# Kernel tuning notes

Measured on AMD Instinct MI355X. Metric: run time of the kernel, lower is better.

The kernel has to match this reference:

```python
import math
import jax, jax.numpy as jnp
import numpy as np

D_MODEL = 1024
N_HEADS = 16
D_FF = 4096
B = 4
T = 1024  # tgt len
S = 1024  # src len
EPS = 1e-6


def _linear_params(key, d_in, d_out):
    kw, kb = jax.random.split(key)
    w = jax.random.normal(kw, (d_out, d_in), dtype=jnp.float32) * 0.02
    b = jax.random.normal(kb, (d_out,), dtype=jnp.float32) * 0.02
    return w, b


def setup_inputs() -> dict:
    key = jax.random.key(0)
    ks = jax.random.split(key, 16)
    x = jax.random.normal(ks[0], (B, T, D_MODEL), dtype=jnp.float32)
    memory = jax.random.normal(ks[1], (B, S, D_MODEL), dtype=jnp.float32)
    # causal [B, T, T] mask (dim==3 branch) and padding [B, S] mask (dim==2 branch)
    tgt_mask = jnp.broadcast_to(jnp.tril(jnp.ones((T, T), dtype=jnp.int32)), (B, T, T))
    src_mask = jnp.ones((B, S), dtype=jnp.int32)
    inp = {"x": x, "memory": memory, "tgt_mask": tgt_mask, "src_mask": src_mask}
    names = ["sa_wq", "sa_wk", "sa_wv", "sa_wo", "ca_wq", "ca_wk", "ca_wv", "ca_wo"]
    for i, n in enumerate(names):
        w, b = _linear_params(ks[2 + i], D_MODEL, D_MODEL)
        inp[n] = w
        inp[n.replace("w", "b")] = b
    inp["ff_w1"], inp["ff_b1"] = _linear_params(ks[10], D_MODEL, D_FF)
    inp["ff_w2"], inp["ff_b2"] = _linear_params(ks[11], D_FF, D_MODEL)
    for i, n in enumerate(["ln1", "ln2", "ln3"]):
        inp[n + "_w"] = jnp.ones((D_MODEL,), dtype=jnp.float32)
        inp[n + "_b"] = jnp.zeros((D_MODEL,), dtype=jnp.float32)
    return inp


def layernorm(x, w, b):
    # torch-faithful: unbiased std (N-1), eps added to std (not variance)
    mean = jnp.mean(x, axis=-1, keepdims=True)
    d = x - mean
    std = jnp.sqrt(jnp.sum(d * d, axis=-1, keepdims=True) / (x.shape[-1] - 1))
    return w * d / (std + EPS) + b


def mha(q_in, kv_in, mask, wq, bq, wk, bk, wv, bv, wo, bo):
    Bb, Tq, D = q_in.shape
    Tk = kv_in.shape[1]
    dk = D // N_HEADS
    if mask.ndim == 2:
        mask4 = mask[:, None, None, :]
    else:
        mask4 = mask[:, None, :, :]
    q = (q_in @ wq.T + bq).reshape(Bb, Tq, N_HEADS, dk).transpose(0, 2, 1, 3)
    k = (kv_in @ wk.T + bk).reshape(Bb, Tk, N_HEADS, dk).transpose(0, 2, 1, 3)
    v = (kv_in @ wv.T + bv).reshape(Bb, Tk, N_HEADS, dk).transpose(0, 2, 1, 3)
    scores = jnp.einsum("bhqd,bhkd->bhqk", q, k) / math.sqrt(dk)
    scores = jnp.where(mask4 == 0, jnp.float32(-1e9), scores)
    attn = jax.nn.softmax(scores, axis=-1)
    out = jnp.einsum("bhqk,bhkd->bhqd", attn, v)
    out = out.transpose(0, 2, 1, 3).reshape(Bb, Tq, D)
    return out @ wo.T + bo


def reference(x, memory, tgt_mask, src_mask,
              sa_wq, sa_bq, sa_wk, sa_bk, sa_wv, sa_bv, sa_wo, sa_bo,
              ca_wq, ca_bq, ca_wk, ca_bk, ca_wv, ca_bv, ca_wo, ca_bo,
              ff_w1, ff_b1, ff_w2, ff_b2,
              ln1_w, ln1_b, ln2_w, ln2_b, ln3_w, ln3_b):
    # pre-norm decoder block (norm_first=True), dropout=0 (eval)
    h = layernorm(x, ln1_w, ln1_b)
    x = x + mha(h, h, tgt_mask, sa_wq, sa_bq, sa_wk, sa_bk, sa_wv, sa_bv, sa_wo, sa_bo)
    h = layernorm(x, ln2_w, ln2_b)
    x = x + mha(h, memory, src_mask, ca_wq, ca_bq, ca_wk, ca_bk, ca_wv, ca_bv, ca_wo, ca_bo)
    h = layernorm(x, ln3_w, ln3_b)
    x = x + (jax.nn.relu(h @ ff_w1.T + ff_b1) @ ff_w2.T + ff_b2)
    return x
```

## Files before the change

kernel.cpp:

```cpp
#include <hip/hip_runtime.h>
#include <hip/hip_bf16.h>

typedef unsigned short u16;
typedef __attribute__((ext_vector_type(4))) float f32x4;
typedef __attribute__((ext_vector_type(8))) short s16x8;
typedef __attribute__((ext_vector_type(4))) short s16x4;
typedef __attribute__((ext_vector_type(8))) __bf16 bf16x8;

#define NTOK 4096
#define DMODEL 1024
#define DFF 4096
#define NH 16
#define TSEQ 1024


__device__ __forceinline__ u16 f2bu(float f) {
  unsigned int u = __float_as_uint(f);
  unsigned int r = (u + 0x7FFFu + ((u >> 16) & 1u)) >> 16;
  return (u16)r;
}

__device__ __forceinline__ f32x4 mfma16(s16x8 a, s16x8 b, f32x4 c) {
  return __builtin_amdgcn_mfma_f32_16x16x32_bf16((bf16x8)a, (bf16x8)b, c, 0, 0, 0);
}

__device__ __forceinline__ void gload16(const u16* g, u16* l) {
  __builtin_amdgcn_global_load_lds(
      (const __attribute__((address_space(1))) unsigned int*)g,
      (__attribute__((address_space(3))) unsigned int*)l, 16, 0, 0);
}

__device__ __forceinline__ s16x8 ldfrag(const u16* p) {
  s16x4 lo = *(const s16x4*)p;
  s16x4 hi = *(const s16x4*)(p + 16);
  s16x8 r;
  r[0] = lo[0]; r[1] = lo[1]; r[2] = lo[2]; r[3] = lo[3];
  r[4] = hi[0]; r[5] = hi[1]; r[6] = hi[2]; r[7] = hi[3];
  return r;
}

__device__ __forceinline__ s16x8 ld8s(const u16* t, int row, int eoff) {
  int rx = row & 7;
  const u16* p1 = t + row * 64 + ((((eoff >> 3) ^ rx) << 3) | (eoff & 7));
  const u16* p2 = t + row * 64 + (((((eoff + 16) >> 3) ^ rx) << 3) | (eoff & 7));
  s16x4 lo = *(const s16x4*)p1;
  s16x4 hi = *(const s16x4*)p2;
  s16x8 r;
  r[0] = lo[0]; r[1] = lo[1]; r[2] = lo[2]; r[3] = lo[3];
  r[4] = hi[0]; r[5] = hi[1]; r[6] = hi[2]; r[7] = hi[3];
  return r;
}

__device__ __forceinline__ s16x8 ld16s(const u16* t, int row, int ch) {
  return *(const s16x8*)(t + row * 64 + ((ch ^ (row & 7)) << 3));
}


struct F2B {
  const float* s[11];
  u16* d[11];
};

__global__ __launch_bounds__(256) void f2b_all(F2B a) {
  int bid = blockIdx.x;
  int seg, boff;
  if (bid < 8192) { seg = bid >> 10; boff = bid & 1023; }
  else { int j = bid - 8192; seg = 8 + (j >> 12); boff = j & 4095; }
  size_t i = ((size_t)boff * 256 + threadIdx.x) * 4;
  float4 v = *(const float4*)(a.s[seg] + i);
  ushort4 o = make_ushort4(f2bu(v.x), f2bu(v.y), f2bu(v.z), f2bu(v.w));
  *(ushort4*)(a.d[seg] + i) = o;
}


__global__ __launch_bounds__(256) void ln_kernel(const float* __restrict__ x,
                                                 const float* __restrict__ w,
                                                 const float* __restrict__ b,
                                                 u16* __restrict__ out) {
  int row = blockIdx.x;
  int t = threadIdx.x;
  const float* xr = x + (size_t)row * DMODEL;
  float4 v = *(const float4*)(xr + t * 4);
  float s = v.x + v.y + v.z + v.w;
#pragma unroll
  for (int off = 1; off < 64; off <<= 1) s += __shfl_xor(s, off);
  __shared__ float red[8];
  int wid = t >> 6, lane = t & 63;
  if (lane == 0) red[wid] = s;
  __syncthreads();
  float mean = (red[0] + red[1] + red[2] + red[3]) * (1.0f / 1024.0f);
  float dx = v.x - mean, dy = v.y - mean, dz = v.z - mean, dw = v.w - mean;
  float ss = dx * dx + dy * dy + dz * dz + dw * dw;
#pragma unroll
  for (int off = 1; off < 64; off <<= 1) ss += __shfl_xor(ss, off);
  if (lane == 0) red[4 + wid] = ss;
  __syncthreads();
  float sst = red[4] + red[5] + red[6] + red[7];
  float inv = 1.0f / (sqrtf(sst / 1023.0f) + 1e-6f);
  float4 wv = *(const float4*)(w + t * 4);
  float4 bv = *(const float4*)(b + t * 4);
  ushort4 o = make_ushort4(f2bu(wv.x * dx * inv + bv.x), f2bu(wv.y * dy * inv + bv.y),
                           f2bu(wv.z * dz * inv + bv.z), f2bu(wv.w * dw * inv + bv.w));
  *(ushort4*)(out + (size_t)row * DMODEL + t * 4) = o;
}


template <int MODE, bool RELU>
__global__ __launch_bounds__(512) void gemm_bt(const u16* __restrict__ A,
                                               const u16* __restrict__ W,
                                               const float* __restrict__ b0,
                                               const float* __restrict__ b1,
                                               const float* __restrict__ b2,
                                               const float* resid, void* outp,
                                               int M, int N, int K, int gx) {
  __shared__ u16 As[2][128 * 64];
  __shared__ u16 Bs[2][128 * 64];
  const int nwg = gridDim.x;
  const int qch = nwg >> 3;
  const int bid = blockIdx.x;
  const int wg = (bid & 7) * qch + (bid >> 3);
  const int bx = wg % gx, by = wg / gx;
  const int m0 = by * 128, n0 = bx * 128;
  const int tid = threadIdx.x;
  const int wid = tid >> 6, lane = tid & 63;
  const int wr = wid >> 2, wc = wid & 3;
  const int lhi = lane >> 4, llo = lane & 15;
  f32x4 acc[4][2] = {};
  const int sr = tid >> 3, sc = tid & 7;
  const int srcoff = (sc ^ (sr & 7)) << 3;

  auto stage = [&](int kk, int buf) {
    const u16* Ap = A + (size_t)(m0 + sr) * K + kk + srcoff;
    gload16(Ap, &As[buf][tid * 8]);
    gload16(Ap + (size_t)64 * K, &As[buf][4096 + tid * 8]);
    const u16* Wp = W + (size_t)(n0 + sr) * K + kk + srcoff;
    gload16(Wp, &Bs[buf][tid * 8]);
    gload16(Wp + (size_t)64 * K, &Bs[buf][4096 + tid * 8]);
  };

  stage(0, 0);
  __syncthreads();

  for (int k0 = 0; k0 < K; k0 += 64) {
    int cur = (k0 >> 6) & 1;
    if (k0 + 64 < K) stage(k0 + 64, cur ^ 1);
#pragma unroll
    for (int ks8 = 0; ks8 < 8; ks8 += 4) {
      s16x8 af[4], bfr[2];
#pragma unroll
      for (int f = 0; f < 4; f++) af[f] = ld16s(&As[cur][0], wr * 64 + f * 16 + llo, ks8 + lhi);
#pragma unroll
      for (int g = 0; g < 2; g++) bfr[g] = ld16s(&Bs[cur][0], wc * 32 + g * 16 + llo, ks8 + lhi);
#pragma unroll
      for (int f = 0; f < 4; f++)
#pragma unroll
        for (int g = 0; g < 2; g++) acc[f][g] = mfma16(af[f], bfr[g], acc[f][g]);
    }
    __syncthreads();
  }

  const float* bias;
  if (MODE == 2) {
    int bs = n0 >> 10;
    bias = (bs == 0) ? b0 : ((bs == 1) ? b1 : b2);
  } else {
    bias = b0;
  }

#pragma unroll
  for (int fm = 0; fm < 4; fm++) {
#pragma unroll
    for (int fn = 0; fn < 2; fn++) {
      int c = n0 + wc * 32 + fn * 16 + llo;
      float bv = (MODE == 2) ? bias[c & 1023] : bias[c];
#pragma unroll
      for (int i = 0; i < 4; i++) {
        int r = m0 + wr * 64 + fm * 16 + lhi * 4 + i;
        float v = acc[fm][fn][i] + bv;
        if (resid) v += resid[(size_t)r * N + c];
        if (RELU) v = fmaxf(v, 0.0f);
        if (MODE == 0) {
          ((float*)outp)[(size_t)r * N + c] = v;
        } else if (MODE == 1) {
          ((u16*)outp)[(size_t)r * N + c] = f2bu(v);
        } else {
          int buf = c >> 10, cc = c & 1023;
          int bb = r >> 10, t = r & 1023, hh = cc >> 6, d = cc & 63;
          ((u16*)outp)[(size_t)buf * 4194304 +
                       (((size_t)(bb * NH + hh)) * TSEQ + t) * 64 + d] = f2bu(v);
        }
      }
    }
  }
}


template <bool CAUSAL>
__global__ __launch_bounds__(256) void attn_kernel(const u16* __restrict__ Qg,
                                                   const u16* __restrict__ Kg,
                                                   const u16* __restrict__ Vg,
                                                   u16* __restrict__ Og) {
  int bh = blockIdx.y;
  int b = bh >> 4, h = bh & 15;
  int q0 = blockIdx.x * 64;
  int tid = threadIdx.x, wid = tid >> 6, lane = tid & 63;
  int lhi = lane >> 4, llo = lane & 15;
  __shared__ u16 Ks[2][4096];
  __shared__ u16 Vs[2][4096];

  int qrow = q0 + wid * 16 + llo;
  const u16* qp = Qg + ((size_t)bh * TSEQ + qrow) * 64;
  s16x8 qf0 = ldfrag(qp + lhi * 4);
  s16x8 qf1 = ldfrag(qp + 32 + lhi * 4);

  f32x4 oacc[4] = {};
  float mrun = -3.0e38f, lrun = 0.0f;
  const size_t kvbase = (size_t)bh * TSEQ * 64;
  const int nt = (CAUSAL ? (q0 + 64) : TSEQ) >> 6;

  const int kr = tid >> 3, kc = tid & 7;
  const int ksrc = (kc ^ (kr & 7)) << 3;
  const int vkv = tid & 63, vd0 = (tid >> 6) * 8;
  s16x8 vr0, vr1;

  auto stageK = [&](int s0, int buf) {
    const u16* kb = Kg + kvbase + (size_t)s0 * 64;
    gload16(kb + (size_t)kr * 64 + ksrc, &Ks[buf][tid * 8]);
    gload16(kb + (size_t)(32 + kr) * 64 + ksrc, &Ks[buf][2048 + tid * 8]);
  };
  auto loadV = [&](int s0) {
    const u16* vb = Vg + kvbase + (size_t)(s0 + vkv) * 64;
    vr0 = *(const s16x8*)(vb + vd0);
    vr1 = *(const s16x8*)(vb + vd0 + 32);
  };
  auto writeV = [&](int buf) {
#pragma unroll
    for (int j = 0; j < 8; j++) {
      int d = vd0 + j;
      Vs[buf][d * 64 + ((((vkv >> 3) ^ (d & 7)) << 3) | (vkv & 7))] = (u16)vr0[j];
      int d2 = d + 32;
      Vs[buf][d2 * 64 + ((((vkv >> 3) ^ (d2 & 7)) << 3) | (vkv & 7))] = (u16)vr1[j];
    }
  };

  stageK(0, 0);
  loadV(0);
  writeV(0);
  __syncthreads();

  for (int t = 0; t < nt; ++t) {
    int cur = t & 1;
    if (t + 1 < nt) {
      stageK((t + 1) * 64, cur ^ 1);
      loadV((t + 1) * 64);
    }
    int s0 = t * 64;

    f32x4 sacc[4] = {};
#pragma unroll
    for (int g = 0; g < 4; g++) {
      int row = g * 16 + llo;
      sacc[g] = mfma16(ld8s(&Ks[cur][0], row, lhi * 4), qf0, sacc[g]);
      sacc[g] = mfma16(ld8s(&Ks[cur][0], row, 32 + lhi * 4), qf1, sacc[g]);
    }

    float sv[16];
    float pmax = -3.0e38f;
#pragma unroll
    for (int g = 0; g < 4; g++)
#pragma unroll
      for (int i = 0; i < 4; i++) {
        float sc = sacc[g][i] * 0.125f;
        if (CAUSAL) {
          int kv = s0 + g * 16 + lhi * 4 + i;
          if (kv > qrow) sc = -1.0e9f;
        }
        sv[g * 4 + i] = sc;
        pmax = fmaxf(pmax, sc);
      }
    pmax = fmaxf(pmax, __shfl_xor(pmax, 16));
    pmax = fmaxf(pmax, __shfl_xor(pmax, 32));
    float mnew = fmaxf(mrun, pmax);
    float alpha = __expf(mrun - mnew);
    float pv[16];
    float ls = 0.0f;
#pragma unroll
    for (int j = 0; j < 16; j++) {
      float p = __expf(sv[j] - mnew);
      pv[j] = p;
      ls += p;
    }
    ls += __shfl_xor(ls, 16);
    ls += __shfl_xor(ls, 32);
    lrun = lrun * alpha + ls;
    mrun = mnew;
#pragma unroll
    for (int g = 0; g < 4; g++) {
      oacc[g][0] *= alpha; oacc[g][1] *= alpha;
      oacc[g][2] *= alpha; oacc[g][3] *= alpha;
    }
    s16x8 pf[2];
#pragma unroll
    for (int kk = 0; kk < 2; kk++)
#pragma unroll
      for (int i2 = 0; i2 < 8; i2++)
        pf[kk][i2] = (short)f2bu(pv[(kk * 2 + (i2 >> 2)) * 4 + (i2 & 3)]);
#pragma unroll
    for (int dg = 0; dg < 4; dg++) {
      int row = dg * 16 + llo;
      oacc[dg] = mfma16(ld8s(&Vs[cur][0], row, lhi * 4), pf[0], oacc[dg]);
      oacc[dg] = mfma16(ld8s(&Vs[cur][0], row, 32 + lhi * 4), pf[1], oacc[dg]);
    }

    if (t + 1 < nt) writeV(cur ^ 1);
    __syncthreads();
  }

  float inv = 1.0f / lrun;
  u16* orow = Og + (size_t)(b * TSEQ + qrow) * DMODEL + h * 64;
#pragma unroll
  for (int dg = 0; dg < 4; dg++)
#pragma unroll
    for (int i = 0; i < 4; i++)
      orow[dg * 16 + lhi * 4 + i] = f2bu(oacc[dg][i] * inv);
}


extern "C" void kernel_launch(void* const* d_in, const int* in_sizes, int n_in,
                              void* d_out, int out_size, void* d_ws, size_t ws_size,
                              hipStream_t stream) {
  const float* x      = (const float*)d_in[0];
  const float* memory = (const float*)d_in[1];
  const float* sa_wq = (const float*)d_in[4];  const float* sa_bq = (const float*)d_in[5];
  const float* sa_wk = (const float*)d_in[6];  const float* sa_bk = (const float*)d_in[7];
  const float* sa_wv = (const float*)d_in[8];  const float* sa_bv = (const float*)d_in[9];
  const float* sa_wo = (const float*)d_in[10]; const float* sa_bo = (const float*)d_in[11];
  const float* ca_wq = (const float*)d_in[12]; const float* ca_bq = (const float*)d_in[13];
  const float* ca_wk = (const float*)d_in[14]; const float* ca_bk = (const float*)d_in[15];
  const float* ca_wv = (const float*)d_in[16]; const float* ca_bv = (const float*)d_in[17];
  const float* ca_wo = (const float*)d_in[18]; const float* ca_bo = (const float*)d_in[19];
  const float* ff_w1 = (const float*)d_in[20]; const float* ff_b1 = (const float*)d_in[21];
  const float* ff_w2 = (const float*)d_in[22]; const float* ff_b2 = (const float*)d_in[23];
  const float* ln1_w = (const float*)d_in[24]; const float* ln1_b = (const float*)d_in[25];
  const float* ln2_w = (const float*)d_in[26]; const float* ln2_b = (const float*)d_in[27];
  const float* ln3_w = (const float*)d_in[28]; const float* ln3_b = (const float*)d_in[29];
  float* out = (float*)d_out;

  char* ws = (char*)d_ws;
  const size_t MB = 1u << 20;
  u16* h_bf   = (u16*)(ws + 0 * MB);
  u16* mem_bf = (u16*)(ws + 8 * MB);
  u16* qb     = (u16*)(ws + 16 * MB);
  u16* kb     = (u16*)(ws + 24 * MB);
  u16* vb     = (u16*)(ws + 32 * MB);
  u16* attnb  = (u16*)(ws + 40 * MB);
  u16* ffmid  = (u16*)(ws + 48 * MB);
  u16* w_sq   = (u16*)(ws + 80 * MB);
  u16* w_sk   = (u16*)(ws + 82 * MB);
  u16* w_sv   = (u16*)(ws + 84 * MB);
  u16* w_so   = (u16*)(ws + 86 * MB);
  u16* w_cq   = (u16*)(ws + 88 * MB);
  u16* w_ck   = (u16*)(ws + 90 * MB);
  u16* w_cv   = (u16*)(ws + 92 * MB);
  u16* w_co   = (u16*)(ws + 94 * MB);
  u16* w_f1   = (u16*)(ws + 96 * MB);
  u16* w_f2   = (u16*)(ws + 104 * MB);

  F2B fa;
  fa.s[0] = sa_wq; fa.d[0] = w_sq;
  fa.s[1] = sa_wk; fa.d[1] = w_sk;
  fa.s[2] = sa_wv; fa.d[2] = w_sv;
  fa.s[3] = sa_wo; fa.d[3] = w_so;
  fa.s[4] = ca_wq; fa.d[4] = w_cq;
  fa.s[5] = ca_wk; fa.d[5] = w_ck;
  fa.s[6] = ca_wv; fa.d[6] = w_cv;
  fa.s[7] = ca_wo; fa.d[7] = w_co;
  fa.s[8] = ff_w1; fa.d[8] = w_f1;
  fa.s[9] = ff_w2; fa.d[9] = w_f2;
  fa.s[10] = memory; fa.d[10] = mem_bf;
  f2b_all<<<20480, 256, 0, stream>>>(fa);

  dim3 gattn(16, 64);

  ln_kernel<<<4096, 256, 0, stream>>>(x, ln1_w, ln1_b, h_bf);
  gemm_bt<2, false><<<768, 512, 0, stream>>>(h_bf, w_sq, sa_bq, sa_bk, sa_bv,
                                             nullptr, qb, NTOK, 3072, DMODEL, 24);
  attn_kernel<true><<<gattn, 256, 0, stream>>>(qb, kb, vb, attnb);
  gemm_bt<0, false><<<256, 512, 0, stream>>>(attnb, w_so, sa_bo, nullptr, nullptr,
                                             x, out, NTOK, DMODEL, DMODEL, 8);

  ln_kernel<<<4096, 256, 0, stream>>>(out, ln2_w, ln2_b, h_bf);
  gemm_bt<2, false><<<256, 512, 0, stream>>>(h_bf, w_cq, ca_bq, nullptr, nullptr,
                                             nullptr, qb, NTOK, DMODEL, DMODEL, 8);
  gemm_bt<2, false><<<512, 512, 0, stream>>>(mem_bf, w_ck, ca_bk, ca_bv, nullptr,
                                             nullptr, kb, NTOK, 2048, DMODEL, 16);
  attn_kernel<false><<<gattn, 256, 0, stream>>>(qb, kb, vb, attnb);
  gemm_bt<0, false><<<256, 512, 0, stream>>>(attnb, w_co, ca_bo, nullptr, nullptr,
                                             out, out, NTOK, DMODEL, DMODEL, 8);

  ln_kernel<<<4096, 256, 0, stream>>>(out, ln3_w, ln3_b, h_bf);
  gemm_bt<1, true><<<1024, 512, 0, stream>>>(h_bf, w_f1, ff_b1, nullptr, nullptr,
                                             nullptr, ffmid, NTOK, DFF, DMODEL, 32);
  gemm_bt<0, false><<<256, 512, 0, stream>>>(ffmid, w_f2, ff_b2, nullptr, nullptr,
                                             out, out, NTOK, DMODEL, DFF, 8);

  (void)in_sizes; (void)n_in; (void)out_size; (void)ws_size;
}
```

Measured before the change: 367.2 us.

## Split-K the FF2 GEMM and process 128 query rows per attention block

The FF2 GEMM (K=4096) is split into two K-halves over 512 workgroups. Each half writes fp32 partials to workspace, and a new reduce kernel sums them and adds bias and residual. The attention kernel now handles two 64-row query tiles per block, so each staged K/V tile is reused twice. Causal blocks skip the first tile where it is fully masked. This adds partial-buffer traffic and an extra launch, plus register pressure from doubled accumulators and halved attention grid parallelism.

```diff
diff --git a/kernel.cpp b/kernel.cpp
--- a/kernel.cpp
+++ b/kernel.cpp
@@ -105,22 +105,26 @@
 }
 
 
-template <int MODE, bool RELU>
+template <int MODE, bool RELU, bool SPLITK = false>
 __global__ __launch_bounds__(512) void gemm_bt(const u16* __restrict__ A,
                                                const u16* __restrict__ W,
                                                const float* __restrict__ b0,
                                                const float* __restrict__ b1,
                                                const float* __restrict__ b2,
                                                const float* resid, void* outp,
-                                               int M, int N, int K, int gx) {
+                                               int M, int N, int K, int ld,
+                                               int gx) {
   __shared__ u16 As[2][128 * 64];
   __shared__ u16 Bs[2][128 * 64];
   const int nwg = gridDim.x;
   const int qch = nwg >> 3;
   const int bid = blockIdx.x;
-  const int wg = (bid & 7) * qch + (bid >> 3);
+  int wg = (bid & 7) * qch + (bid >> 3);
+  int half = 0;
+  if (SPLITK) { half = wg & 1; wg >>= 1; }
   const int bx = wg % gx, by = wg / gx;
   const int m0 = by * 128, n0 = bx * 128;
+  if (SPLITK) { A += (size_t)half * K; W += (size_t)half * K; }
   const int tid = threadIdx.x;
   const int wid = tid >> 6, lane = tid & 63;
   const int wr = wid >> 2, wc = wid & 3;
@@ -130,12 +134,12 @@
   const int srcoff = (sc ^ (sr & 7)) << 3;
 
   auto stage = [&](int kk, int buf) {
-    const u16* Ap = A + (size_t)(m0 + sr) * K + kk + srcoff;
+    const u16* Ap = A + (size_t)(m0 + sr) * ld + kk + srcoff;
     gload16(Ap, &As[buf][tid * 8]);
-    gload16(Ap + (size_t)64 * K, &As[buf][4096 + tid * 8]);
-    const u16* Wp = W + (size_t)(n0 + sr) * K + kk + srcoff;
+    gload16(Ap + (size_t)64 * ld, &As[buf][4096 + tid * 8]);
+    const u16* Wp = W + (size_t)(n0 + sr) * ld + kk + srcoff;
     gload16(Wp, &Bs[buf][tid * 8]);
-    gload16(Wp + (size_t)64 * K, &Bs[buf][4096 + tid * 8]);
+    gload16(Wp + (size_t)64 * ld, &Bs[buf][4096 + tid * 8]);
   };
 
   stage(0, 0);
@@ -172,7 +176,7 @@
 #pragma unroll
     for (int fn = 0; fn < 2; fn++) {
       int c = n0 + wc * 32 + fn * 16 + llo;
-      float bv = (MODE == 2) ? bias[c & 1023] : bias[c];
+      float bv = bias ? (MODE == 2 ? bias[c & 1023] : bias[c]) : 0.0f;
 #pragma unroll
       for (int i = 0; i < 4; i++) {
         int r = m0 + wr * 64 + fm * 16 + lhi * 4 + i;
@@ -180,7 +184,7 @@
         if (resid) v += resid[(size_t)r * N + c];
         if (RELU) v = fmaxf(v, 0.0f);
         if (MODE == 0) {
-          ((float*)outp)[(size_t)r * N + c] = v;
+          ((float*)outp)[(size_t)half * M * N + (size_t)r * N + c] = v;
         } else if (MODE == 1) {
           ((u16*)outp)[(size_t)r * N + c] = f2bu(v);
         } else {
@@ -195,6 +199,22 @@
 }
 
 
+__global__ __launch_bounds__(256) void ff2_reduce(const float* __restrict__ p,
+                                                  const float* __restrict__ bias,
+                                                  float* __restrict__ out) {
+  int row = blockIdx.x, t = threadIdx.x;
+  size_t i = (size_t)row * 1024 + t * 4;
+  const float* p1 = p + (size_t)4194304;
+  float4 a = *(const float4*)(p + i);
+  float4 b = *(const float4*)(p1 + i);
+  float4 r = *(const float4*)(out + i);
+  float4 bv = *(const float4*)(bias + t * 4);
+  float4 o = make_float4(a.x + b.x + r.x + bv.x, a.y + b.y + r.y + bv.y,
+                         a.z + b.z + r.z + bv.z, a.w + b.w + r.w + bv.w);
+  *(float4*)(out + i) = o;
+}
+
+
 template <bool CAUSAL>
 __global__ __launch_bounds__(256) void attn_kernel(const u16* __restrict__ Qg,
                                                    const u16* __restrict__ Kg,
@@ -202,21 +222,25 @@
                                                    u16* __restrict__ Og) {
   int bh = blockIdx.y;
   int b = bh >> 4, h = bh & 15;
-  int q0 = blockIdx.x * 64;
+  int q0 = blockIdx.x * 128;
   int tid = threadIdx.x, wid = tid >> 6, lane = tid & 63;
   int lhi = lane >> 4, llo = lane & 15;
   __shared__ u16 Ks[2][4096];
   __shared__ u16 Vs[2][4096];
 
-  int qrow = q0 + wid * 16 + llo;
-  const u16* qp = Qg + ((size_t)bh * TSEQ + qrow) * 64;
-  s16x8 qf0 = ldfrag(qp + lhi * 4);
-  s16x8 qf1 = ldfrag(qp + 32 + lhi * 4);
-
-  f32x4 oacc[4] = {};
-  float mrun = -3.0e38f, lrun = 0.0f;
+  int qr = q0 + wid * 16 + llo;
+  const u16* qp0 = Qg + ((size_t)bh * TSEQ + qr) * 64;
+  const u16* qp1 = qp0 + 64 * 64;
+  s16x8 qf[2][2];
+  qf[0][0] = ldfrag(qp0 + lhi * 4);
+  qf[0][1] = ldfrag(qp0 + 32 + lhi * 4);
+  qf[1][0] = ldfrag(qp1 + lhi * 4);
+  qf[1][1] = ldfrag(qp1 + 32 + lhi * 4);
+
+  f32x4 oacc[2][4] = {};
+  float mrun[2] = {-3.0e38f, -3.0e38f}, lrun[2] = {0.0f, 0.0f};
   const size_t kvbase = (size_t)bh * TSEQ * 64;
-  const int nt = (CAUSAL ? (q0 + 64) : TSEQ) >> 6;
+  const int nt = (CAUSAL ? (q0 + 128) : TSEQ) >> 6;
 
   const int kr = tid >> 3, kc = tid & 7;
   const int ksrc = (kc ^ (kr & 7)) << 3;
@@ -255,74 +279,95 @@
       loadV((t + 1) * 64);
     }
     int s0 = t * 64;
-
-    f32x4 sacc[4] = {};
+    const bool act0 = !CAUSAL || (s0 < q0 + 64);
+
+    s16x8 kf[4][2];
 #pragma unroll
     for (int g = 0; g < 4; g++) {
       int row = g * 16 + llo;
-      sacc[g] = mfma16(ld8s(&Ks[cur][0], row, lhi * 4), qf0, sacc[g]);
-      sacc[g] = mfma16(ld8s(&Ks[cur][0], row, 32 + lhi * 4), qf1, sacc[g]);
-    }
-
-    float sv[16];
-    float pmax = -3.0e38f;
-#pragma unroll
-    for (int g = 0; g < 4; g++)
-#pragma unroll
-      for (int i = 0; i < 4; i++) {
-        float sc = sacc[g][i] * 0.125f;
-        if (CAUSAL) {
-          int kv = s0 + g * 16 + lhi * 4 + i;
-          if (kv > qrow) sc = -1.0e9f;
+      kf[g][0] = ld8s(&Ks[cur][0], row, lhi * 4);
+      kf[g][1] = ld8s(&Ks[cur][0], row, 32 + lhi * 4);
+    }
+
+    s16x8 pf[2][2];
+#pragma unroll
+    for (int s = 0; s < 2; s++) {
+      if (s == 0 && !act0) continue;
+      f32x4 sacc[4] = {};
+#pragma unroll
+      for (int g = 0; g < 4; g++) {
+        sacc[g] = mfma16(kf[g][0], qf[s][0], sacc[g]);
+        sacc[g] = mfma16(kf[g][1], qf[s][1], sacc[g]);
+      }
+      int qrow = qr + s * 64;
+      float sv[16];
+      float pmax = -3.0e38f;
+#pragma unroll
+      for (int g = 0; g < 4; g++)
+#pragma unroll
+        for (int i = 0; i < 4; i++) {
+          float sc = sacc[g][i] * 0.125f;
+          if (CAUSAL) {
+            int kv = s0 + g * 16 + lhi * 4 + i;
+            if (kv > qrow) sc = -1.0e9f;
+          }
+          sv[g * 4 + i] = sc;
+          pmax = fmaxf(pmax, sc);
         }
-        sv[g * 4 + i] = sc;
-        pmax = fmaxf(pmax, sc);
+      pmax = fmaxf(pmax, __shfl_xor(pmax, 16));
+      pmax = fmaxf(pmax, __shfl_xor(pmax, 32));
+      float mnew = fmaxf(mrun[s], pmax);
+      float alpha = __expf(mrun[s] - mnew);
+      float ls = 0.0f;
+#pragma unroll
+      for (int j = 0; j < 16; j++) {
+        float p = __expf(sv[j] - mnew);
+        sv[j] = p;
+        ls += p;
       }
-    pmax = fmaxf(pmax, __shfl_xor(pmax, 16));
-    pmax = fmaxf(pmax, __shfl_xor(pmax, 32));
-    float mnew = fmaxf(mrun, pmax);
-    float alpha = __expf(mrun - mnew);
-    float pv[16];
-    float ls = 0.0f;
-#pragma unroll
-    for (int j = 0; j < 16; j++) {
-      float p = __expf(sv[j] - mnew);
-      pv[j] = p;
-      ls += p;
-    }
-    ls += __shfl_xor(ls, 16);
-    ls += __shfl_xor(ls, 32);
-    lrun = lrun * alpha + ls;
-    mrun = mnew;
-#pragma unroll
-    for (int g = 0; g < 4; g++) {
-      oacc[g][0] *= alpha; oacc[g][1] *= alpha;
-      oacc[g][2] *= alpha; oacc[g][3] *= alpha;
-    }
-    s16x8 pf[2];
-#pragma unroll
-    for (int kk = 0; kk < 2; kk++)
-#pragma unroll
-      for (int i2 = 0; i2 < 8; i2++)
-        pf[kk][i2] = (short)f2bu(pv[(kk * 2 + (i2 >> 2)) * 4 + (i2 & 3)]);
+      ls += __shfl_xor(ls, 16);
+      ls += __shfl_xor(ls, 32);
+      lrun[s] = lrun[s] * alpha + ls;
+      mrun[s] = mnew;
+#pragma unroll
+      for (int g = 0; g < 4; g++) {
+        oacc[s][g][0] *= alpha; oacc[s][g][1] *= alpha;
+        oacc[s][g][2] *= alpha; oacc[s][g][3] *= alpha;
+      }
+#pragma unroll
+      for (int kk = 0; kk < 2; kk++)
+#pragma unroll
+        for (int i2 = 0; i2 < 8; i2++)
+          pf[s][kk][i2] = (short)f2bu(sv[(kk * 2 + (i2 >> 2)) * 4 + (i2 & 3)]);
+    }
+
 #pragma unroll
     for (int dg = 0; dg < 4; dg++) {
       int row = dg * 16 + llo;
-      oacc[dg] = mfma16(ld8s(&Vs[cur][0], row, lhi * 4), pf[0], oacc[dg]);
-      oacc[dg] = mfma16(ld8s(&Vs[cur][0], row, 32 + lhi * 4), pf[1], oacc[dg]);
+      s16x8 vf0 = ld8s(&Vs[cur][0], row, lhi * 4);
+      s16x8 vf1 = ld8s(&Vs[cur][0], row, 32 + lhi * 4);
+#pragma unroll
+      for (int s = 0; s < 2; s++) {
+        if (s == 0 && !act0) continue;
+        oacc[s][dg] = mfma16(vf0, pf[s][0], oacc[s][dg]);
+        oacc[s][dg] = mfma16(vf1, pf[s][1], oacc[s][dg]);
+      }
     }
 
     if (t + 1 < nt) writeV(cur ^ 1);
     __syncthreads();
   }
 
-  float inv = 1.0f / lrun;
-  u16* orow = Og + (size_t)(b * TSEQ + qrow) * DMODEL + h * 64;
-#pragma unroll
-  for (int dg = 0; dg < 4; dg++)
-#pragma unroll
-    for (int i = 0; i < 4; i++)
-      orow[dg * 16 + lhi * 4 + i] = f2bu(oacc[dg][i] * inv);
+#pragma unroll
+  for (int s = 0; s < 2; s++) {
+    float inv = 1.0f / lrun[s];
+    u16* orow = Og + (size_t)(b * TSEQ + qr + s * 64) * DMODEL + h * 64;
+#pragma unroll
+    for (int dg = 0; dg < 4; dg++)
+#pragma unroll
+      for (int i = 0; i < 4; i++)
+        orow[dg * 16 + lhi * 4 + i] = f2bu(oacc[s][dg][i] * inv);
+  }
 }
 
 
@@ -355,6 +400,7 @@
   u16* vb     = (u16*)(ws + 32 * MB);
   u16* attnb  = (u16*)(ws + 40 * MB);
   u16* ffmid  = (u16*)(ws + 48 * MB);
+  float* pk   = (float*)(ws + 16 * MB);
   u16* w_sq   = (u16*)(ws + 80 * MB);
   u16* w_sk   = (u16*)(ws + 82 * MB);
   u16* w_sv   = (u16*)(ws + 84 * MB);
@@ -380,29 +426,30 @@
   fa.s[10] = memory; fa.d[10] = mem_bf;
   f2b_all<<<20480, 256, 0, stream>>>(fa);
 
-  dim3 gattn(16, 64);
+  dim3 gattn(8, 64);
 
   ln_kernel<<<4096, 256, 0, stream>>>(x, ln1_w, ln1_b, h_bf);
   gemm_bt<2, false><<<768, 512, 0, stream>>>(h_bf, w_sq, sa_bq, sa_bk, sa_bv,
-                                             nullptr, qb, NTOK, 3072, DMODEL, 24);
+                                             nullptr, qb, NTOK, 3072, DMODEL, DMODEL, 24);
   attn_kernel<true><<<gattn, 256, 0, stream>>>(qb, kb, vb, attnb);
   gemm_bt<0, false><<<256, 512, 0, stream>>>(attnb, w_so, sa_bo, nullptr, nullptr,
-                                             x, out, NTOK, DMODEL, DMODEL, 8);
+                                             x, out, NTOK, DMODEL, DMODEL, DMODEL, 8);
 
   ln_kernel<<<4096, 256, 0, stream>>>(out, ln2_w, ln2_b, h_bf);
   gemm_bt<2, false><<<256, 512, 0, stream>>>(h_bf, w_cq, ca_bq, nullptr, nullptr,
-                                             nullptr, qb, NTOK, DMODEL, DMODEL, 8);
+                                             nullptr, qb, NTOK, DMODEL, DMODEL, DMODEL, 8);
   gemm_bt<2, false><<<512, 512, 0, stream>>>(mem_bf, w_ck, ca_bk, ca_bv, nullptr,
-                                             nullptr, kb, NTOK, 2048, DMODEL, 16);
+                                             nullptr, kb, NTOK, 2048, DMODEL, DMODEL, 16);
   attn_kernel<false><<<gattn, 256, 0, stream>>>(qb, kb, vb, attnb);
   gemm_bt<0, false><<<256, 512, 0, stream>>>(attnb, w_co, ca_bo, nullptr, nullptr,
-                                             out, out, NTOK, DMODEL, DMODEL, 8);
+                                             out, out, NTOK, DMODEL, DMODEL, DMODEL, 8);
 
   ln_kernel<<<4096, 256, 0, stream>>>(out, ln3_w, ln3_b, h_bf);
   gemm_bt<1, true><<<1024, 512, 0, stream>>>(h_bf, w_f1, ff_b1, nullptr, nullptr,
-                                             nullptr, ffmid, NTOK, DFF, DMODEL, 32);
-  gemm_bt<0, false><<<256, 512, 0, stream>>>(ffmid, w_f2, ff_b2, nullptr, nullptr,
-                                             out, out, NTOK, DMODEL, DFF, 8);
+                                             nullptr, ffmid, NTOK, DFF, DMODEL, DMODEL, 32);
+  gemm_bt<0, false, true><<<512, 512, 0, stream>>>(ffmid, w_f2, nullptr, nullptr, nullptr,
+                                                   nullptr, pk, NTOK, DMODEL, 2048, DFF, 8);
+  ff2_reduce<<<4096, 256, 0, stream>>>(pk, ff_b2, out);
 
   (void)in_sizes; (void)n_in; (void)out_size; (void)ws_size;
 }
```

After: 353.9 us. -3.6%, faster.
